# Optimization experiments

Measured on AMD Instinct MI355X. Metric: run time of the kernel, lower is better.

## Reference

```python
import jax, jax.numpy as jnp
import numpy as np

NEG_SLOPE = 0.2


def setup_inputs() -> dict:
    key = jax.random.key(0)
    ks = jax.random.split(key, 7)
    N, E, IN, H, D = 100000, 1000000, 256, 4, 32
    feat = jax.random.normal(ks[0], (N, IN), dtype=jnp.float32)
    W_fc = jax.random.normal(ks[1], (H * D, IN), dtype=jnp.float32) * (1.0 / np.sqrt(IN))
    attn_l = jax.random.normal(ks[2], (1, H, D), dtype=jnp.float32) * 0.1
    attn_r = jax.random.normal(ks[3], (1, H, D), dtype=jnp.float32) * 0.1
    bias = jnp.zeros((H * D,), dtype=jnp.float32)
    src = jax.random.randint(ks[4], (E,), 0, N, dtype=jnp.int32)
    dst = jax.random.randint(ks[5], (E,), 0, N, dtype=jnp.int32)
    return {"feat": feat, "W_fc": W_fc, "attn_l": attn_l, "attn_r": attn_r, "bias": bias, "src": src, "dst": dst}


def reference(feat, W_fc, attn_l, attn_r, bias, src, dst):
    N = feat.shape[0]
    H, D = attn_l.shape[1], attn_l.shape[2]
    # fc projection; note: in the non-tuple path the module uses self.fc for
    # BOTH feat_src and feat_src2, so they are identical.
    h = (feat @ W_fc.T).reshape(N, H, D)  # [N,H,D]
    el = jnp.sum(h * attn_l, axis=-1)  # [N,H]
    er = jnpp_sum = jnp.sum(h * attn_r, axis=-1)  # [N,H]
    e = jax.nn.leaky_relu(el[src] + er[dst], NEG_SLOPE)  # [E,H]
    # edge softmax normalized over incoming edges of each dst node
    e_max = jax.ops.segment_max(e, dst, num_segments=N)  # [N,H]
    ex = jnp.exp(e - e_max[dst])
    denom = jax.ops.segment_sum(ex, dst, num_segments=N)  # [N,H]
    a = ex / denom[dst]  # [E,H]
    # attention-weighted aggregation: sum_e a_e * h[src_e] -> dst
    initial_ft = jax.ops.segment_sum(h[src] * a[:, :, None], dst, num_segments=N)
    # second path: u_mul_v then sum to dst (feat_src2 == feat_dst2 == h)
    add_ft = jax.ops.segment_sum(h[src] * h[dst], dst, num_segments=N)
    rst = initial_ft + add_ft + bias.reshape(1, H, D)
    return rst
```

## Files before the change

kernel.cpp:

```cpp
#include <hip/hip_runtime.h>
#include <hip/hip_bf16.h>
#include <hip/hip_fp16.h>
#include <math.h>

#define NEG_SLOPE 0.2f

typedef __attribute__((ext_vector_type(8))) short short8v;
typedef __attribute__((ext_vector_type(4))) float f32x4;

__device__ __forceinline__ float uas(unsigned int u) { return __uint_as_float(u); }

__device__ __forceinline__ unsigned short f2bf(float x) {
    __hip_bfloat16 b = __float2bfloat16(x);
    return *(unsigned short*)&b;
}

__global__ void k_prep(const float* __restrict__ W, const float* __restrict__ al,
                       const float* __restrict__ ar, short* __restrict__ wfrag) {
    int p = blockIdx.x * 256 + threadIdx.x;
    if (p >= 144 * 32) return;
    int n = p >> 5, kg = p & 31;
    float v[8];
    if (n < 128) {
        const float* wp = W + (size_t)n * 256 + kg * 8;
        float4 v0 = *(const float4*)wp;
        float4 v1 = *(const float4*)(wp + 4);
        v[0] = v0.x; v[1] = v0.y; v[2] = v0.z; v[3] = v0.w;
        v[4] = v1.x; v[5] = v1.y; v[6] = v1.z; v[7] = v1.w;
    } else if (n < 136) {
        int i = n - 128, hh = i & 3, lr = i >> 2;
        const float* av = lr ? ar : al;
#pragma unroll
        for (int j = 0; j < 8; j++) v[j] = 0.f;
        for (int c = 0; c < 32; c++) {
            float a = av[hh * 32 + c];
            const float* wp = W + (size_t)(hh * 32 + c) * 256 + kg * 8;
#pragma unroll
            for (int j = 0; j < 8; j++) v[j] += a * wp[j];
        }
    } else {
#pragma unroll
        for (int j = 0; j < 8; j++) v[j] = 0.f;
    }
    short s8[8];
#pragma unroll
    for (int j = 0; j < 8; j++) s8[j] = (short)f2bf(v[j]);
    int kstep = kg >> 2, ntile = n >> 4;
    int L     = (kg & 3) * 16 + (n & 15);
    int slot  = kstep * 9 + ntile;
    *(short8v*)&wfrag[(slot * 64 + L) * 8] = *(short8v*)s8;
}

__global__ __launch_bounds__(256) void k_gemm(const float* __restrict__ feat,
                                              const short* __restrict__ wfrag,
                                              unsigned short* __restrict__ hb,
                                              float* __restrict__ el,
                                              float* __restrict__ er, int N) {
    __shared__ short wlds[32768];
    const int t    = threadIdx.x;
    const int lane = t & 63;
    const int wave = t >> 6;
    const int n0   = blockIdx.x * 64;
    const int g    = lane >> 4;
    const int c    = lane & 15;

#pragma unroll
    for (int i = 0; i < 16; i++) {
        int p  = t + i * 256;
        int sl = p >> 6, li = p & 63;
        int gs = (sl >> 3) * 9 + (sl & 7);
        *(short8v*)&wlds[(size_t)p * 8] =
            *(const short8v*)&wfrag[((size_t)gs * 64 + li) * 8];
    }

    const int row = n0 + wave * 16 + c;
    const int rc  = row < N ? row : N - 1;
    const float* ap = feat + (size_t)rc * 256 + g * 8;
    float4 a4[16];
#pragma unroll
    for (int ks = 0; ks < 8; ks++) {
        a4[2 * ks]     = *(const float4*)(ap + ks * 32);
        a4[2 * ks + 1] = *(const float4*)(ap + ks * 32 + 4);
    }

    __syncthreads();

    f32x4 acc[9];
#pragma unroll
    for (int nt = 0; nt < 9; nt++) acc[nt] = (f32x4){0.f, 0.f, 0.f, 0.f};

#pragma unroll
    for (int ks = 0; ks < 8; ks++) {
        float4 v0 = a4[2 * ks], v1 = a4[2 * ks + 1];
        short s8[8];
        s8[0] = (short)f2bf(v0.x); s8[1] = (short)f2bf(v0.y);
        s8[2] = (short)f2bf(v0.z); s8[3] = (short)f2bf(v0.w);
        s8[4] = (short)f2bf(v1.x); s8[5] = (short)f2bf(v1.y);
        s8[6] = (short)f2bf(v1.z); s8[7] = (short)f2bf(v1.w);
        short8v afrag = *(short8v*)s8;
        short8v b8 = *(const short8v*)&wfrag[(((size_t)ks * 9 + 8) * 64 + lane) * 8];
#pragma unroll
        for (int nt = 0; nt < 8; nt++) {
            short8v b = *(short8v*)&wlds[(((size_t)ks * 8 + nt) * 64 + lane) * 8];
            acc[nt] = __builtin_amdgcn_mfma_f32_16x16x32_bf16(afrag, b, acc[nt], 0, 0, 0);
        }
        acc[8] = __builtin_amdgcn_mfma_f32_16x16x32_bf16(afrag, b8, acc[8], 0, 0, 0);
    }

#pragma unroll
    for (int r = 0; r < 4; r++) {
        int m = n0 + wave * 16 + g * 4 + r;
        if (m < N) {
#pragma unroll
            for (int nt = 0; nt < 8; nt++)
                hb[(size_t)m * 128 + nt * 16 + c] = f2bf(acc[nt][r]);
            float av = acc[8][r];
            if (c < 4)      el[(size_t)m * 4 + c]       = av;
            else if (c < 8) er[(size_t)m * 4 + (c - 4)] = av;
        }
    }
}

#define NPB_SHIFT 8
#define BIN_EPT   16
#define BIN_EDGES (256 * BIN_EPT)

__global__ __launch_bounds__(256) void k_binhist(const int* __restrict__ dst,
                                                 int* __restrict__ bcount,
                                                 int E, int NB) {
    __shared__ int hist[512];
    int t = threadIdx.x;
    for (int i = t; i < NB; i += 256) hist[i] = 0;
    __syncthreads();
    int base = blockIdx.x * BIN_EDGES + t;
#pragma unroll
    for (int k = 0; k < BIN_EPT; k++) {
        int idx = base + k * 256;
        if (idx < E) atomicAdd(&hist[dst[idx] >> NPB_SHIFT], 1);
    }
    __syncthreads();
    for (int i = t; i < NB; i += 256) {
        int h = hist[i];
        if (h) atomicAdd(&bcount[i], h);
    }
}

__global__ __launch_bounds__(512) void k_bscan(const int* __restrict__ bcount,
                                               int* __restrict__ bbase,
                                               int* __restrict__ bcur, int NB) {
    __shared__ int s[512];
    int t = threadIdx.x;
    int h = (t < NB) ? bcount[t] : 0;
    s[t] = h;
    __syncthreads();
    for (int off = 1; off < 512; off <<= 1) {
        int v = (t >= off) ? s[t - off] : 0;
        __syncthreads();
        s[t] += v;
        __syncthreads();
    }
    int excl = s[t] - h;
    if (t <= NB) bbase[t] = excl;
    if (t < NB)  bcur[t]  = excl;
}

__global__ __launch_bounds__(256) void k_binscatter(const int* __restrict__ src,
                                                    const int* __restrict__ dst,
                                                    int* __restrict__ bcur,
                                                    int2* __restrict__ binned,
                                                    int E, int NB) {
    __shared__ int hist[512];
    __shared__ int cur[512];
    int t = threadIdx.x;
    for (int i = t; i < NB; i += 256) hist[i] = 0;
    __syncthreads();
    int base = blockIdx.x * BIN_EDGES + t;
    int sv[BIN_EPT], dv[BIN_EPT];
#pragma unroll
    for (int k = 0; k < BIN_EPT; k++) {
        int idx = base + k * 256;
        if (idx < E) {
            sv[k] = src[idx];
            dv[k] = dst[idx];
            atomicAdd(&hist[dv[k] >> NPB_SHIFT], 1);
        } else {
            dv[k] = -1;
        }
    }
    __syncthreads();
    for (int i = t; i < NB; i += 256) {
        int h = hist[i];
        cur[i] = h ? atomicAdd(&bcur[i], h) : 0;
    }
    __syncthreads();
#pragma unroll
    for (int k = 0; k < BIN_EPT; k++) {
        if (dv[k] >= 0) {
            int p = atomicAdd(&cur[dv[k] >> NPB_SHIFT], 1);
            binned[p] = make_int2(sv[k], dv[k]);
        }
    }
}

__global__ __launch_bounds__(256) void k_csr(const int2* __restrict__ binned,
                                             const int* __restrict__ bbase,
                                             int* __restrict__ startA,
                                             int* __restrict__ deg,
                                             int* __restrict__ src_csr, int N) {
    __shared__ int hist[256];
    __shared__ int scn[256];
    __shared__ int cur[256];
    int b = blockIdx.x;
    int t = threadIdx.x;
    int base = bbase[b];
    int cnt  = bbase[b + 1] - base;
    int node0 = b << NPB_SHIFT;
    hist[t] = 0;
    __syncthreads();
    for (int i = t; i < cnt; i += 256) {
        int2 e = binned[base + i];
        atomicAdd(&hist[e.y - node0], 1);
    }
    __syncthreads();
    int h = hist[t];
    scn[t] = h;
    __syncthreads();
    for (int off = 1; off < 256; off <<= 1) {
        int v = (t >= off) ? scn[t - off] : 0;
        __syncthreads();
        scn[t] += v;
        __syncthreads();
    }
    int excl  = scn[t] - h;
    int gnode = node0 + t;
    if (gnode < N) { deg[gnode] = h; startA[gnode] = base + excl; }
    cur[t] = excl;
    __syncthreads();
    for (int i = t; i < cnt; i += 256) {
        int2 e = binned[base + i];
        int p = atomicAdd(&cur[e.y - node0], 1);
        src_csr[base + p] = e.x;
    }
}

__global__ __launch_bounds__(256) void k_agg(
        const unsigned int* __restrict__ hbu,
        const float* __restrict__ el, const float* __restrict__ er,
        const int* __restrict__ src_csr,
        const int* __restrict__ start, const int* __restrict__ deg,
        const float* __restrict__ bias, float* __restrict__ out, int N) {
    int wid  = blockIdx.x * 4 + (threadIdx.x >> 6);
    int lane = threadIdx.x & 63;
    if (wid >= N) return;
    int beg = __builtin_amdgcn_readfirstlane(start[wid]);
    int dg  = __builtin_amdgcn_readfirstlane(deg[wid]);
    int head = lane >> 4;

    float er_own = er[(size_t)wid * 4 + head];

    float S1x = 0.f, S1y = 0.f, S2x = 0.f, S2y = 0.f, dd = 0.f;
    int i = 0;
    for (; i + 4 <= dg; i += 4) {
        int b = beg + i;
        int s0 = src_csr[b], s1 = src_csr[b + 1], s2 = src_csr[b + 2], s3 = src_csr[b + 3];
        unsigned int u0 = hbu[(size_t)s0 * 64 + lane];
        unsigned int u1 = hbu[(size_t)s1 * 64 + lane];
        unsigned int u2 = hbu[(size_t)s2 * 64 + lane];
        unsigned int u3 = hbu[(size_t)s3 * 64 + lane];
        float t0 = el[(size_t)s0 * 4 + head] + er_own;
        float t1 = el[(size_t)s1 * 4 + head] + er_own;
        float t2 = el[(size_t)s2 * 4 + head] + er_own;
        float t3 = el[(size_t)s3 * 4 + head] + er_own;
        t0 = t0 > 0.f ? t0 : NEG_SLOPE * t0;
        t1 = t1 > 0.f ? t1 : NEG_SLOPE * t1;
        t2 = t2 > 0.f ? t2 : NEG_SLOPE * t2;
        t3 = t3 > 0.f ? t3 : NEG_SLOPE * t3;
        float w0 = __expf(t0), w1 = __expf(t1), w2 = __expf(t2), w3 = __expf(t3);
        float x0 = uas(u0 << 16), y0 = uas(u0 & 0xFFFF0000u);
        float x1 = uas(u1 << 16), y1 = uas(u1 & 0xFFFF0000u);
        float x2 = uas(u2 << 16), y2 = uas(u2 & 0xFFFF0000u);
        float x3 = uas(u3 << 16), y3 = uas(u3 & 0xFFFF0000u);
        S1x += (x0 + x1) + (x2 + x3);
        S1y += (y0 + y1) + (y2 + y3);
        S2x += w0 * x0 + w1 * x1 + w2 * x2 + w3 * x3;
        S2y += w0 * y0 + w1 * y1 + w2 * y2 + w3 * y3;
        dd  += (w0 + w1) + (w2 + w3);
    }
    for (; i < dg; i++) {
        int b = beg + i;
        int s0 = src_csr[b];
        unsigned int u0 = hbu[(size_t)s0 * 64 + lane];
        float t0 = el[(size_t)s0 * 4 + head] + er_own;
        t0 = t0 > 0.f ? t0 : NEG_SLOPE * t0;
        float w0 = __expf(t0);
        float x0 = uas(u0 << 16), y0 = uas(u0 & 0xFFFF0000u);
        S1x += x0; S1y += y0;
        S2x += w0 * x0; S2y += w0 * y0;
        dd  += w0;
    }

    unsigned int uh = hbu[(size_t)wid * 64 + lane];
    float hvx = uas(uh << 16), hvy = uas(uh & 0xFFFF0000u);
    float2 bv = ((const float2*)bias)[lane];
    float inv = dd > 0.f ? 1.f / dd : 0.f;
    float ox = bv.x + hvx * S1x + S2x * inv;
    float oy = bv.y + hvy * S1y + S2y * inv;
    float2 o = {ox, oy};
    ((float2*)(out + (size_t)wid * 128))[lane] = o;
}

extern "C" void kernel_launch(void* const* d_in, const int* in_sizes, int n_in,
                              void* d_out, int out_size, void* d_ws, size_t ws_size,
                              hipStream_t stream) {
    const float* feat = (const float*)d_in[0];
    const float* W_fc = (const float*)d_in[1];
    const float* al   = (const float*)d_in[2];
    const float* ar   = (const float*)d_in[3];
    const float* bias = (const float*)d_in[4];
    const int*   src  = (const int*)d_in[5];
    const int*   dst  = (const int*)d_in[6];
    const int N = in_sizes[0] / 256;
    const int E = in_sizes[5];
    const int NB = (N + 255) >> NPB_SHIFT;

    char* ws = (char*)d_ws;
    size_t off = 0;
    unsigned int* hbu = (unsigned int*)(ws + off); off += (size_t)N * 64 * 4;
    float* el         = (float*)(ws + off); off += (size_t)N * 4 * 4;
    float* er         = (float*)(ws + off); off += (size_t)N * 4 * 4;
    int* deg          = (int*)(ws + off);   off += (size_t)N * 4;
    int* startA       = (int*)(ws + off);   off += (size_t)N * 4;
    int* src_csr      = (int*)(ws + off);   off += (size_t)E * 4;
    int2* binned      = (int2*)(ws + off);  off += (size_t)E * 8;
    short* wfrag      = (short*)(ws + off); off += (size_t)72 * 64 * 8 * 2;
    int* bcount       = (int*)(ws + off);   off += 2048;
    int* bbase        = (int*)(ws + off);   off += 2064;
    int* bcur         = (int*)(ws + off);   off += 2048;

    float* out = (float*)d_out;

    hipMemsetAsync(bcount, 0, (size_t)NB * 4, stream);
    k_prep<<<18, 256, 0, stream>>>(W_fc, al, ar, wfrag);
    k_gemm<<<(N + 63) / 64, 256, 0, stream>>>(feat, wfrag, (unsigned short*)hbu,
                                              el, er, N);
    int binWG = (E + BIN_EDGES - 1) / BIN_EDGES;
    k_binhist<<<binWG, 256, 0, stream>>>(dst, bcount, E, NB);
    k_bscan<<<1, 512, 0, stream>>>(bcount, bbase, bcur, NB);
    k_binscatter<<<binWG, 256, 0, stream>>>(src, dst, bcur, binned, E, NB);
    k_csr<<<NB, 256, 0, stream>>>(binned, bbase, startA, deg, src_csr, N);
    k_agg<<<(N + 3) / 4, 256, 0, stream>>>(hbu, el, er, src_csr, startA, deg,
                                           bias, out, N);
}
```

Measured before the change: 290.7 us.

## Fuse bin histogram into GEMM, drop memset, pack binned edges to 32 bits

Moves the destination-bin histogram into the tail of the GEMM kernel, with the first 245 GEMM blocks each also counting one chunk of edges. The bcount zeroing moves into k_prep, so one memset and one kernel launch go away. Binned edges are packed into one 32-bit word (24-bit src, 8-bit local dst), which halves the traffic for the scatter and CSR passes. The packing assumes N fits in 24 bits, and the histogram work adds load imbalance to the GEMM blocks that take part.

```diff
diff --git a/kernel.cpp b/kernel.cpp
--- a/kernel.cpp
+++ b/kernel.cpp
@@ -15,9 +15,15 @@
     return *(unsigned short*)&b;
 }
 
+#define NPB_SHIFT 8
+#define BIN_EPT   16
+#define BIN_EDGES (256 * BIN_EPT)
+
 __global__ void k_prep(const float* __restrict__ W, const float* __restrict__ al,
-                       const float* __restrict__ ar, short* __restrict__ wfrag) {
+                       const float* __restrict__ ar, short* __restrict__ wfrag,
+                       int* __restrict__ bcount, int NB) {
     int p = blockIdx.x * 256 + threadIdx.x;
+    if (p < NB) bcount[p] = 0;
     if (p >= 144 * 32) return;
     int n = p >> 5, kg = p & 31;
     float v[8];
@@ -55,14 +61,23 @@
                                               const short* __restrict__ wfrag,
                                               unsigned short* __restrict__ hb,
                                               float* __restrict__ el,
-                                              float* __restrict__ er, int N) {
+                                              float* __restrict__ er, int N,
+                                              const int* __restrict__ dst,
+                                              int* __restrict__ bcount,
+                                              int E, int NB) {
     __shared__ short wlds[32768];
+    __shared__ int bh[512];
     const int t    = threadIdx.x;
     const int lane = t & 63;
     const int wave = t >> 6;
     const int n0   = blockIdx.x * 64;
     const int g    = lane >> 4;
     const int c    = lane & 15;
+    const bool do_hist = (blockIdx.x * BIN_EDGES) < E;
+
+    if (do_hist) {
+        for (int i = t; i < 512; i += 256) bh[i] = 0;
+    }
 
 #pragma unroll
     for (int i = 0; i < 16; i++) {
@@ -119,29 +134,19 @@
             else if (c < 8) er[(size_t)m * 4 + (c - 4)] = av;
         }
     }
-}
-
-#define NPB_SHIFT 8
-#define BIN_EPT   16
-#define BIN_EDGES (256 * BIN_EPT)
-
-__global__ __launch_bounds__(256) void k_binhist(const int* __restrict__ dst,
-                                                 int* __restrict__ bcount,
-                                                 int E, int NB) {
-    __shared__ int hist[512];
-    int t = threadIdx.x;
-    for (int i = t; i < NB; i += 256) hist[i] = 0;
-    __syncthreads();
-    int base = blockIdx.x * BIN_EDGES + t;
-#pragma unroll
-    for (int k = 0; k < BIN_EPT; k++) {
-        int idx = base + k * 256;
-        if (idx < E) atomicAdd(&hist[dst[idx] >> NPB_SHIFT], 1);
-    }
-    __syncthreads();
-    for (int i = t; i < NB; i += 256) {
-        int h = hist[i];
-        if (h) atomicAdd(&bcount[i], h);
+
+    if (do_hist) {
+        int base = blockIdx.x * BIN_EDGES + t;
+#pragma unroll
+        for (int k = 0; k < BIN_EPT; k++) {
+            int idx = base + k * 256;
+            if (idx < E) atomicAdd(&bh[dst[idx] >> NPB_SHIFT], 1);
+        }
+        __syncthreads();
+        for (int i = t; i < NB; i += 256) {
+            int h = bh[i];
+            if (h) atomicAdd(&bcount[i], h);
+        }
     }
 }
 
@@ -167,7 +172,7 @@
 __global__ __launch_bounds__(256) void k_binscatter(const int* __restrict__ src,
                                                     const int* __restrict__ dst,
                                                     int* __restrict__ bcur,
-                                                    int2* __restrict__ binned,
+                                                    unsigned int* __restrict__ binned,
                                                     int E, int NB) {
     __shared__ int hist[512];
     __shared__ int cur[512];
@@ -197,12 +202,12 @@
     for (int k = 0; k < BIN_EPT; k++) {
         if (dv[k] >= 0) {
             int p = atomicAdd(&cur[dv[k] >> NPB_SHIFT], 1);
-            binned[p] = make_int2(sv[k], dv[k]);
-        }
-    }
-}
-
-__global__ __launch_bounds__(256) void k_csr(const int2* __restrict__ binned,
+            binned[p] = (unsigned int)sv[k] | ((unsigned int)(dv[k] & 255) << 24);
+        }
+    }
+}
+
+__global__ __launch_bounds__(256) void k_csr(const unsigned int* __restrict__ binned,
                                              const int* __restrict__ bbase,
                                              int* __restrict__ startA,
                                              int* __restrict__ deg,
@@ -218,8 +223,8 @@
     hist[t] = 0;
     __syncthreads();
     for (int i = t; i < cnt; i += 256) {
-        int2 e = binned[base + i];
-        atomicAdd(&hist[e.y - node0], 1);
+        unsigned int e = binned[base + i];
+        atomicAdd(&hist[e >> 24], 1);
     }
     __syncthreads();
     int h = hist[t];
@@ -237,9 +242,9 @@
     cur[t] = excl;
     __syncthreads();
     for (int i = t; i < cnt; i += 256) {
-        int2 e = binned[base + i];
-        int p = atomicAdd(&cur[e.y - node0], 1);
-        src_csr[base + p] = e.x;
+        unsigned int e = binned[base + i];
+        int p = atomicAdd(&cur[e >> 24], 1);
+        src_csr[base + p] = (int)(e & 0xFFFFFFu);
     }
 }
 
@@ -331,7 +336,7 @@
     int* deg          = (int*)(ws + off);   off += (size_t)N * 4;
     int* startA       = (int*)(ws + off);   off += (size_t)N * 4;
     int* src_csr      = (int*)(ws + off);   off += (size_t)E * 4;
-    int2* binned      = (int2*)(ws + off);  off += (size_t)E * 8;
+    unsigned int* binned = (unsigned int*)(ws + off); off += (size_t)E * 4;
     short* wfrag      = (short*)(ws + off); off += (size_t)72 * 64 * 8 * 2;
     int* bcount       = (int*)(ws + off);   off += 2048;
     int* bbase        = (int*)(ws + off);   off += 2064;
@@ -339,12 +344,10 @@
 
     float* out = (float*)d_out;
 
-    hipMemsetAsync(bcount, 0, (size_t)NB * 4, stream);
-    k_prep<<<18, 256, 0, stream>>>(W_fc, al, ar, wfrag);
+    k_prep<<<18, 256, 0, stream>>>(W_fc, al, ar, wfrag, bcount, NB);
     k_gemm<<<(N + 63) / 64, 256, 0, stream>>>(feat, wfrag, (unsigned short*)hbu,
-                                              el, er, N);
+                                              el, er, N, dst, bcount, E, NB);
     int binWG = (E + BIN_EDGES - 1) / BIN_EDGES;
-    k_binhist<<<binWG, 256, 0, stream>>>(dst, bcount, E, NB);
     k_bscan<<<1, 512, 0, stream>>>(bcount, bbase, bcur, NB);
     k_binscatter<<<binWG, 256, 0, stream>>>(src, dst, bcur, binned, E, NB);
     k_csr<<<NB, 256, 0, stream>>>(binned, bbase, startA, deg, src_csr, N);
```

Measured after the change: 273.7 us. 5.8% less time.
